# Performance work log

Measured on AMD Instinct MI355X. Metric: run time of the kernel, lower is better.

Reference implementation:

```python
import jax, jax.numpy as jnp
import numpy as np

E = 1_000_000
D_IN = 64
D_OUT = 64
N_TYPES = 8


def setup_inputs() -> dict:
    key = jax.random.key(0)
    k1, k2, k3, k4 = jax.random.split(key, 4)
    edge_features = jax.random.normal(k1, (E, D_IN), dtype=jnp.float32)
    edge_types = jax.random.randint(k2, (E,), 0, N_TYPES, dtype=jnp.int64)
    # per-type Linear params: W[t] is [in, out], b[t] is [out]
    W = jax.random.normal(k3, (N_TYPES, D_IN, D_OUT), dtype=jnp.float32) * (1.0 / np.sqrt(D_IN))
    b = jax.random.normal(k4, (N_TYPES, D_OUT), dtype=jnp.float32) * 0.01
    return {"edge_features": edge_features, "edge_types": edge_types, "W": W, "b": b}


def reference(edge_features, edge_types, W, b):
    # Per-edge-type Linear + ReLU, scattered back by type mask.
    # Loop is over the small fixed set of edge types (structurally distinct
    # weight matrices), not over the edge data dimension.
    out = jnp.zeros((edge_features.shape[0], D_OUT), dtype=edge_features.dtype)
    for t in range(N_TYPES):
        y = jax.nn.relu(edge_features @ W[t] + b[t])  # [E, D_OUT]
        mask = (edge_types == t)[:, None]
        out = jnp.where(mask, y, out)
    return out
```

## Files before the change

### kernel.cpp

```cpp
#include <hip/hip_runtime.h>
#include <stdint.h>

#define D 64
#define NT 8
#define CHUNK 1024
#define BLOCK 256

typedef __attribute__((ext_vector_type(8))) short short8;
typedef __attribute__((ext_vector_type(4))) float f32x4;

__device__ __forceinline__ unsigned short f2bf(float f) {
    union { float f; unsigned u; } v; v.f = f;
    unsigned u = v.u;
    unsigned r = (u + 0x7FFFu + ((u >> 16) & 1u)) >> 16;
    return (unsigned short)r;
}

__global__ void __launch_bounds__(BLOCK)
edge_mlp_kernel(const float* __restrict__ ef, const int* __restrict__ types,
                const float* __restrict__ W, const float* __restrict__ Bv,
                float* __restrict__ out, int E)
{
    __shared__ unsigned short bucket[CHUNK];
    __shared__ unsigned cnt[NT];
    __shared__ unsigned startoff[NT];
    __shared__ unsigned cursor[NT];

    const int tid  = threadIdx.x;
    const int base = blockIdx.x * CHUNK;
    const int clen = min(CHUNK, E - base);
    if (clen <= 0) return;

    if (tid < NT) cnt[tid] = 0;
    __syncthreads();

    int myt[CHUNK / BLOCK];
#pragma unroll
    for (int i = 0; i < CHUNK / BLOCK; ++i) {
        int idx = tid + i * BLOCK;
        int t = -1;
        if (idx < clen) {
            t = types[base + idx];
            atomicAdd(&cnt[t], 1u);
        }
        myt[i] = t;
    }
    __syncthreads();
    if (tid == 0) {
        unsigned s = 0;
        for (int t = 0; t < NT; ++t) { startoff[t] = s; cursor[t] = s; s += cnt[t]; }
    }
    __syncthreads();
#pragma unroll
    for (int i = 0; i < CHUNK / BLOCK; ++i) {
        if (myt[i] >= 0) {
            unsigned pos = atomicAdd(&cursor[myt[i]], 1u);
            bucket[pos] = (unsigned short)(tid + i * BLOCK);
        }
    }
    __syncthreads();

    const int wave = tid >> 6;
    const int lane = tid & 63;
    const int n = lane & 15;
    const int g = lane >> 4;

    for (int ti = 0; ti < 2; ++ti) {
        const int t = wave * 2 + ti;
        const unsigned V  = cnt[t];
        if (V == 0) continue;
        const unsigned bs = startoff[t];

        short8 bf[2][4];
        const float* Wt = W + (size_t)t * D * D;
#pragma unroll
        for (int kb = 0; kb < 2; ++kb) {
#pragma unroll
            for (int nb = 0; nb < 4; ++nb) {
                short8 f;
#pragma unroll
                for (int j = 0; j < 8; ++j) {
                    float w = Wt[(size_t)(kb * 32 + g * 8 + j) * D + nb * 16 + n];
                    f[j] = (short)f2bf(w);
                }
                bf[kb][nb] = f;
            }
        }
        float bias[4];
#pragma unroll
        for (int nb = 0; nb < 4; ++nb) bias[nb] = Bv[t * D + nb * 16 + n];

        const unsigned nbatch = (V + 15u) >> 4;
        for (unsigned b = 0; b < nbatch; ++b) {
            const unsigned p0 = b << 4;
            unsigned pm = p0 + (unsigned)n;
            if (pm >= V) pm = V - 1;
            const int gidx = base + (int)bucket[bs + pm];
            const float* row = ef + (size_t)gidx * D;

            f32x4 a0 = *(const f32x4*)(row + g * 8);
            f32x4 a1 = *(const f32x4*)(row + g * 8 + 4);
            f32x4 a2 = *(const f32x4*)(row + 32 + g * 8);
            f32x4 a3 = *(const f32x4*)(row + 32 + g * 8 + 4);

            short8 fa0, fa1;
#pragma unroll
            for (int j = 0; j < 4; ++j) {
                fa0[j]     = (short)f2bf(a0[j]);
                fa0[j + 4] = (short)f2bf(a1[j]);
                fa1[j]     = (short)f2bf(a2[j]);
                fa1[j + 4] = (short)f2bf(a3[j]);
            }

            f32x4 acc[4];
#pragma unroll
            for (int nb = 0; nb < 4; ++nb) acc[nb] = (f32x4){0.f, 0.f, 0.f, 0.f};

#pragma unroll
            for (int nb = 0; nb < 4; ++nb) {
                acc[nb] = __builtin_amdgcn_mfma_f32_16x16x32_bf16(fa0, bf[0][nb], acc[nb], 0, 0, 0);
                acc[nb] = __builtin_amdgcn_mfma_f32_16x16x32_bf16(fa1, bf[1][nb], acc[nb], 0, 0, 0);
            }

#pragma unroll
            for (int r = 0; r < 4; ++r) {
                const int rowpos = g * 4 + r;
                const int sidx = __shfl(gidx, rowpos);
                if (p0 + (unsigned)rowpos < V) {
                    float* orow = out + (size_t)sidx * D;
#pragma unroll
                    for (int nb = 0; nb < 4; ++nb) {
                        float v = acc[nb][r] + bias[nb];
                        orow[nb * 16 + n] = v > 0.f ? v : 0.f;
                    }
                }
            }
        }
    }
}

extern "C" void kernel_launch(void* const* d_in, const int* in_sizes, int n_in,
                              void* d_out, int out_size, void* d_ws, size_t ws_size,
                              hipStream_t stream) {
    const float* ef    = (const float*)d_in[0];
    const int*   types = (const int*)d_in[1];
    const float* W     = (const float*)d_in[2];
    const float* Bv    = (const float*)d_in[3];
    float* out = (float*)d_out;
    const int E = in_sizes[1];
    const int grid = (E + CHUNK - 1) / CHUNK;
    hipLaunchKernelGGL(edge_mlp_kernel, dim3(grid), dim3(BLOCK), 0, stream,
                       ef, types, W, Bv, out, E);
}
```

Measured before the change: 446.1 us.

## Replace per-type bucketing with dense masked MFMA over all types per tile

Drops the shared-memory type bucketing and scattered gather/store. Each wave now processes contiguous 64-edge tiles and runs MFMAs for all 8 types, zeroing A fragments for rows of other types so results accumulate correctly. All weights are staged once per block in LDS as swizzled packed bf16, using the hardware pack-convert instruction, and the occupancy hint is raised. This gives fully coalesced loads and stores in exchange for 8x the MFMA work and a large LDS footprint.

```diff
diff --git a/kernel.cpp b/kernel.cpp
--- a/kernel.cpp
+++ b/kernel.cpp
@@ -3,60 +3,46 @@
 
 #define D 64
 #define NT 8
-#define CHUNK 1024
 #define BLOCK 256
+#define TPB 16
 
 typedef __attribute__((ext_vector_type(8))) short short8;
 typedef __attribute__((ext_vector_type(4))) float f32x4;
 
-__device__ __forceinline__ unsigned short f2bf(float f) {
-    union { float f; unsigned u; } v; v.f = f;
-    unsigned u = v.u;
-    unsigned r = (u + 0x7FFFu + ((u >> 16) & 1u)) >> 16;
-    return (unsigned short)r;
+__device__ __forceinline__ unsigned pkbf(float lo, float hi) {
+    unsigned r;
+    asm("v_cvt_pk_bf16_f32 %0, %1, %2" : "=v"(r) : "v"(lo), "v"(hi));
+    return r;
 }
 
-__global__ void __launch_bounds__(BLOCK)
+__global__ void __launch_bounds__(BLOCK, 2)
 edge_mlp_kernel(const float* __restrict__ ef, const int* __restrict__ types,
                 const float* __restrict__ W, const float* __restrict__ Bv,
                 float* __restrict__ out, int E)
 {
-    __shared__ unsigned short bucket[CHUNK];
-    __shared__ unsigned cnt[NT];
-    __shared__ unsigned startoff[NT];
-    __shared__ unsigned cursor[NT];
+    __shared__ unsigned WT[NT * 2048];
+    __shared__ float BIAS[NT * D];
 
-    const int tid  = threadIdx.x;
-    const int base = blockIdx.x * CHUNK;
-    const int clen = min(CHUNK, E - base);
-    if (clen <= 0) return;
+    const int tid = threadIdx.x;
 
-    if (tid < NT) cnt[tid] = 0;
-    __syncthreads();
-
-    int myt[CHUNK / BLOCK];
+    {
+        const int t  = tid >> 5;
+        const int k0 = (tid & 31) * 2;
+        const float* w0 = W + (size_t)t * (D * D) + (size_t)k0 * D;
 #pragma unroll
-    for (int i = 0; i < CHUNK / BLOCK; ++i) {
-        int idx = tid + i * BLOCK;
-        int t = -1;
-        if (idx < clen) {
-            t = types[base + idx];
-            atomicAdd(&cnt[t], 1u);
+        for (int c4 = 0; c4 < D; c4 += 4) {
+            f32x4 ra = *(const f32x4*)(w0 + c4);
+            f32x4 rb = *(const f32x4*)(w0 + D + c4);
+#pragma unroll
+            for (int j = 0; j < 4; ++j) {
+                const int c = c4 + j;
+                unsigned idx = (unsigned)(t * 2048 + c * 32 + (k0 >> 1));
+                idx ^= (unsigned)((c & 7) << 2);
+                WT[idx] = pkbf(ra[j], rb[j]);
+            }
         }
-        myt[i] = t;
-    }
-    __syncthreads();
-    if (tid == 0) {
-        unsigned s = 0;
-        for (int t = 0; t < NT; ++t) { startoff[t] = s; cursor[t] = s; s += cnt[t]; }
-    }
-    __syncthreads();
-#pragma unroll
-    for (int i = 0; i < CHUNK / BLOCK; ++i) {
-        if (myt[i] >= 0) {
-            unsigned pos = atomicAdd(&cursor[myt[i]], 1u);
-            bucket[pos] = (unsigned short)(tid + i * BLOCK);
-        }
+        BIAS[tid]       = Bv[tid];
+        BIAS[tid + 256] = Bv[tid + 256];
     }
     __syncthreads();
 
@@ -64,73 +50,90 @@
     const int lane = tid & 63;
     const int n = lane & 15;
     const int g = lane >> 4;
+    const int ntiles = (E + 63) >> 6;
 
-    for (int ti = 0; ti < 2; ++ti) {
-        const int t = wave * 2 + ti;
-        const unsigned V  = cnt[t];
-        if (V == 0) continue;
-        const unsigned bs = startoff[t];
+    for (int it = 0; it < 4; ++it) {
+        const int ti = blockIdx.x * TPB + wave * 4 + it;
+        if (ti >= ntiles) break;
+        const int tb = ti << 6;
 
-        short8 bf[2][4];
-        const float* Wt = W + (size_t)t * D * D;
+        int eidx = tb + lane; if (eidx >= E) eidx = E - 1;
+        const int t_lane = types[eidx];
+
+        f32x4 a[4][4];
 #pragma unroll
-        for (int kb = 0; kb < 2; ++kb) {
+        for (int mt = 0; mt < 4; ++mt) {
+            int row = tb + mt * 16 + n; if (row >= E) row = E - 1;
+            const float* rp = ef + (size_t)row * D + g * 8;
+            a[mt][0] = *(const f32x4*)(rp);
+            a[mt][1] = *(const f32x4*)(rp + 4);
+            a[mt][2] = *(const f32x4*)(rp + 32);
+            a[mt][3] = *(const f32x4*)(rp + 36);
+        }
+
+        short8 fa[4][2];
 #pragma unroll
-            for (int nb = 0; nb < 4; ++nb) {
-                short8 f;
+        for (int mt = 0; mt < 4; ++mt) {
+            union { unsigned u[4]; short8 s; } u0, u1;
+            u0.u[0] = pkbf(a[mt][0][0], a[mt][0][1]);
+            u0.u[1] = pkbf(a[mt][0][2], a[mt][0][3]);
+            u0.u[2] = pkbf(a[mt][1][0], a[mt][1][1]);
+            u0.u[3] = pkbf(a[mt][1][2], a[mt][1][3]);
+            u1.u[0] = pkbf(a[mt][2][0], a[mt][2][1]);
+            u1.u[1] = pkbf(a[mt][2][2], a[mt][2][3]);
+            u1.u[2] = pkbf(a[mt][3][0], a[mt][3][1]);
+            u1.u[3] = pkbf(a[mt][3][2], a[mt][3][3]);
+            fa[mt][0] = u0.s;
+            fa[mt][1] = u1.s;
+        }
+
+        int tt[4];
 #pragma unroll
-                for (int j = 0; j < 8; ++j) {
-                    float w = Wt[(size_t)(kb * 32 + g * 8 + j) * D + nb * 16 + n];
-                    f[j] = (short)f2bf(w);
+        for (int mt = 0; mt < 4; ++mt) tt[mt] = __shfl(t_lane, mt * 16 + n);
+
+        f32x4 acc[4][4];
+#pragma unroll
+        for (int mt = 0; mt < 4; ++mt)
+#pragma unroll
+            for (int nb = 0; nb < 4; ++nb) acc[mt][nb] = (f32x4){0.f, 0.f, 0.f, 0.f};
+
+        for (int t = 0; t < NT; ++t) {
+            short8 bf[2][4];
+#pragma unroll
+            for (int kb = 0; kb < 2; ++kb)
+#pragma unroll
+                for (int nb = 0; nb < 4; ++nb) {
+                    const int col = nb * 16 + n;
+                    unsigned idx = (unsigned)(t * 2048 + col * 32 + kb * 16 + g * 4);
+                    idx ^= (unsigned)((col & 7) << 2);
+                    bf[kb][nb] = *(const short8*)&WT[idx];
                 }
-                bf[kb][nb] = f;
+            const short8 z = (short8)0;
+#pragma unroll
+            for (int mt = 0; mt < 4; ++mt) {
+                const bool m = (tt[mt] == t);
+                short8 ma0 = m ? fa[mt][0] : z;
+                short8 ma1 = m ? fa[mt][1] : z;
+#pragma unroll
+                for (int nb = 0; nb < 4; ++nb) {
+                    acc[mt][nb] = __builtin_amdgcn_mfma_f32_16x16x32_bf16(ma0, bf[0][nb], acc[mt][nb], 0, 0, 0);
+                    acc[mt][nb] = __builtin_amdgcn_mfma_f32_16x16x32_bf16(ma1, bf[1][nb], acc[mt][nb], 0, 0, 0);
+                }
             }
         }
-        float bias[4];
-#pragma unroll
-        for (int nb = 0; nb < 4; ++nb) bias[nb] = Bv[t * D + nb * 16 + n];
-
-        const unsigned nbatch = (V + 15u) >> 4;
-        for (unsigned b = 0; b < nbatch; ++b) {
-            const unsigned p0 = b << 4;
-            unsigned pm = p0 + (unsigned)n;
-            if (pm >= V) pm = V - 1;
-            const int gidx = base + (int)bucket[bs + pm];
-            const float* row = ef + (size_t)gidx * D;
-
-            f32x4 a0 = *(const f32x4*)(row + g * 8);
-            f32x4 a1 = *(const f32x4*)(row + g * 8 + 4);
-            f32x4 a2 = *(const f32x4*)(row + 32 + g * 8);
-            f32x4 a3 = *(const f32x4*)(row + 32 + g * 8 + 4);
-
-            short8 fa0, fa1;
-#pragma unroll
-            for (int j = 0; j < 4; ++j) {
-                fa0[j]     = (short)f2bf(a0[j]);
-                fa0[j + 4] = (short)f2bf(a1[j]);
-                fa1[j]     = (short)f2bf(a2[j]);
-                fa1[j + 4] = (short)f2bf(a3[j]);
-            }
-
-            f32x4 acc[4];
-#pragma unroll
-            for (int nb = 0; nb < 4; ++nb) acc[nb] = (f32x4){0.f, 0.f, 0.f, 0.f};
 
 #pragma unroll
-            for (int nb = 0; nb < 4; ++nb) {
-                acc[nb] = __builtin_amdgcn_mfma_f32_16x16x32_bf16(fa0, bf[0][nb], acc[nb], 0, 0, 0);
-                acc[nb] = __builtin_amdgcn_mfma_f32_16x16x32_bf16(fa1, bf[1][nb], acc[nb], 0, 0, 0);
-            }
-
+        for (int mt = 0; mt < 4; ++mt) {
 #pragma unroll
             for (int r = 0; r < 4; ++r) {
-                const int rowpos = g * 4 + r;
-                const int sidx = __shfl(gidx, rowpos);
-                if (p0 + (unsigned)rowpos < V) {
-                    float* orow = out + (size_t)sidx * D;
+                const int lrow = mt * 16 + g * 4 + r;
+                const int row  = tb + lrow;
+                const int trow = __shfl(t_lane, lrow);
+                if (row < E) {
+                    float* orow = out + (size_t)row * D;
 #pragma unroll
                     for (int nb = 0; nb < 4; ++nb) {
-                        float v = acc[nb][r] + bias[nb];
+                        float v = acc[mt][nb][r] + BIAS[trow * D + nb * 16 + n];
                         orow[nb * 16 + n] = v > 0.f ? v : 0.f;
                     }
                 }
@@ -148,7 +151,8 @@
     const float* Bv    = (const float*)d_in[3];
     float* out = (float*)d_out;
     const int E = in_sizes[1];
-    const int grid = (E + CHUNK - 1) / CHUNK;
+    const int ntiles = (E + 63) / 64;
+    const int grid = (ntiles + TPB - 1) / TPB;
     hipLaunchKernelGGL(edge_mlp_kernel, dim3(grid), dim3(BLOCK), 0, stream,
                        ef, types, W, Bv, out, E);
 }
```

New measurement: 447.3 us. About the same (+0.3%).
